# Kernel optimization log

Measured on AMD Instinct MI355X. Metric: run time of the kernel, lower is better.

Reference implementation:

```python
import jax, jax.numpy as jnp
import numpy as np

N_NODES = 50000
N_EDGES = 600000
DIM = 128
VOCAB = 512
PAD_ID = 0
LN_EPS = 1e-5


def setup_inputs() -> dict:
    key = jax.random.key(0)
    ks = jax.random.split(key, 8)
    node_ids = jax.random.randint(ks[0], (N_NODES,), 0, VOCAB, dtype=jnp.int32)
    edge_index = jax.random.randint(ks[1], (2, N_EDGES), 0, N_NODES, dtype=jnp.int32)
    edge_weight = jax.random.uniform(ks[2], (N_EDGES,), dtype=jnp.float32)
    # embedding with padding row zeroed (padding_idx semantics)
    emb = jax.random.normal(ks[3], (VOCAB, DIM), dtype=jnp.float32) * 0.05
    emb = emb.at[PAD_ID].set(0.0)
    s = 1.0 / np.sqrt(DIM)
    W1 = jax.random.normal(ks[4], (DIM, DIM), dtype=jnp.float32) * s
    b1 = jnp.zeros((DIM,), jnp.float32)
    W2 = jax.random.normal(ks[5], (DIM, DIM), dtype=jnp.float32) * s
    b2 = jnp.zeros((DIM,), jnp.float32)
    return {
        "node_ids": node_ids, "edge_index": edge_index, "edge_weight": edge_weight,
        "emb": emb, "W1": W1, "b1": b1, "W2": W2, "b2": b2,
        "gamma1": jnp.ones((DIM,), jnp.float32), "beta1": jnp.zeros((DIM,), jnp.float32),
        "gamma2": jnp.ones((DIM,), jnp.float32), "beta2": jnp.zeros((DIM,), jnp.float32),
    }


def _gcn_conv(x, row, col, ew, W, b, n_nodes):
    """PyG GCNConv: normalize=True, add_self_loops=True, improved=False.
    Aggregation j->i: edge (row=src j, col=dst i)."""
    h = x @ W  # [N, out]
    # add self loops with weight 1
    loop = jnp.arange(n_nodes, dtype=row.dtype)
    row_f = jnp.concatenate([row, loop])
    col_f = jnp.concatenate([col, loop])
    ew_f = jnp.concatenate([ew, jnp.ones((n_nodes,), ew.dtype)])
    # symmetric degree normalization (deg over destination index)
    deg = jax.ops.segment_sum(ew_f, col_f, num_segments=n_nodes)
    dis = jnp.where(deg > 0, jax.lax.rsqrt(jnp.maximum(deg, 1e-12)), 0.0)
    norm = dis[row_f] * ew_f * dis[col_f]  # [E+N]
    msg = norm[:, None] * h[row_f]  # gather + scale  [E+N, out]
    out = jax.ops.segment_sum(msg, col_f, num_segments=n_nodes)  # scatter-add
    return out + b


def _layer_norm(x, gamma, beta):
    mu = jnp.mean(x, axis=-1, keepdims=True)
    var = jnp.mean(jnp.square(x - mu), axis=-1, keepdims=True)
    return (x - mu) * jax.lax.rsqrt(var + LN_EPS) * gamma + beta


def reference(node_ids, edge_index, edge_weight, emb, W1, b1, W2, b2,
              gamma1, beta1, gamma2, beta2):
    row, col = edge_index[0], edge_index[1]
    x = emb[node_ids]  # [N, D]
    x1 = _gcn_conv(x, row, col, edge_weight, W1, b1, N_NODES)
    x = _layer_norm(x + x1, gamma1, beta1)  # dropout is identity in eval
    x2 = _gcn_conv(x, row, col, edge_weight, W2, b2, N_NODES)
    x = _layer_norm(x + x2, gamma2, beta2)
    return x
```

## Files before the change

kernel.cpp:

```cpp
#include <hip/hip_runtime.h>

#define N_NODES 50000
#define N_EDGES 600000
#define DIM     128
#define VOCAB   512
#define LN_EPS  1e-5f
#define FIX20   1048576.0f
#define WSC     65535.0f
#define BCAP    64

typedef unsigned int uint;
typedef unsigned long long ull;
typedef unsigned short ushort;
typedef __attribute__((ext_vector_type(8))) short s8v;
typedef __attribute__((ext_vector_type(4))) float f4v;
typedef __attribute__((ext_vector_type(4))) int   i4v;
typedef __attribute__((ext_vector_type(4))) float fv4;
typedef __attribute__((ext_vector_type(2))) float f2v;

__device__ __forceinline__ uint f2bf(float f) {
    uint u = __float_as_uint(f);
    return (u + 0x7fffu + ((u >> 16) & 1u)) >> 16;
}
__device__ __forceinline__ float bf_lo(uint p) { return __uint_as_float(p << 16); }
__device__ __forceinline__ float bf_hi(uint p) { return __uint_as_float(p & 0xffff0000u); }
__device__ __forceinline__ float dis_of(uint pv) {
    return rsqrtf(1.0f + (float)(pv & 0x03ffffffu) * (1.0f / FIX20));
}

__global__ __launch_bounds__(256) void deg_mm1_kernel(
        const int* __restrict__ ei, const float* __restrict__ ew,
        uint2* pairN, const int* __restrict__ nid, uint* __restrict__ epack, int E,
        const float* __restrict__ X, const float* __restrict__ W,
        uint* __restrict__ Hb, int M,
        const float* __restrict__ W2, ushort* __restrict__ Wp) {
    __shared__ float Wt[32 * 128];
    __shared__ float Xt[64 * 36];
    int tid = threadIdx.x;
    int nbDeg = (E / 4 + 255) / 256;
    int nmm = (M + 63) / 64;
    if ((int)blockIdx.x < nbDeg) {
        int e0 = (blockIdx.x * 256 + tid) * 4;
        if (e0 >= E) return;
        i4v s4 = __builtin_nontemporal_load((const i4v*)(ei + e0));
        i4v c4 = __builtin_nontemporal_load((const i4v*)(ei + E + e0));
        fv4 w4 = __builtin_nontemporal_load((const fv4*)(ew + e0));
        int   s[4] = {s4.x, s4.y, s4.z, s4.w};
        int   c[4] = {c4.x, c4.y, c4.z, c4.w};
        float w[4] = {w4.x, w4.y, w4.z, w4.w};
        uint r[4];
        #pragma unroll
        for (int k = 0; k < 4; k++) {
            uint a = (1u << 26) | (uint)__float2int_rn(w[k] * FIX20);
            r[k] = atomicAdd(&((uint*)pairN)[2 * (size_t)c[k]], a);
        }
        #pragma unroll
        for (int k = 0; k < 4; k++) {
            uint rk = r[k] >> 26;
            uint wq = (uint)__float2int_rn(w[k] * WSC);
            epack[(size_t)c[k] * BCAP + rk] = (uint)s[k] | (wq << 16);
        }
        return;
    }
    if ((int)blockIdx.x >= nbDeg + nmm) {
        int o = (blockIdx.x - nbDeg - nmm) * 256 + tid;
        if (o < 16384) {
            int j = o & 7, lane = (o >> 3) & 63, chunk = o >> 9;
            int kc = chunk & 3, nc = chunk >> 2;
            int k = kc * 32 + (lane >> 4) * 8 + j;
            int n = nc * 16 + (lane & 15);
            Wp[o] = (ushort)f2bf(W2[k * 128 + n]);
        } else {
            int i = o - 16384;
            if (i < N_NODES) ((uint*)pairN)[2 * (size_t)i + 1] = (uint)nid[i];
        }
        return;
    }
    int bx = blockIdx.x - nbDeg;
    int tx = tid & 31, ty = tid >> 5;
    int r0 = bx * 64;
    float acc[8][4];
    #pragma unroll
    for (int j = 0; j < 8; j++)
        #pragma unroll
        for (int c = 0; c < 4; c++) acc[j][c] = 0.f;

    for (int kb = 0; kb < 128; kb += 32) {
        __syncthreads();
        #pragma unroll
        for (int q = 0; q < 4; q++) {
            int f = q * 256 + tid;
            ((float4*)Wt)[f] = *(const float4*)(W + kb * 128 + f * 4);
        }
        #pragma unroll
        for (int q = 0; q < 2; q++) {
            int f = q * 256 + tid;
            int row = f >> 3, cs = f & 7;
            int gr = r0 + row;
            float4 xv = make_float4(0.f, 0.f, 0.f, 0.f);
            if (gr < M) xv = *(const float4*)(X + (size_t)gr * 128 + kb + cs * 4);
            *(float4*)(Xt + row * 36 + cs * 4) = xv;
        }
        __syncthreads();
        #pragma unroll
        for (int k = 0; k < 32; k += 4) {
            float wv[4][4];
            #pragma unroll
            for (int kk = 0; kk < 4; kk++) {
                float4 t4 = *(const float4*)(Wt + (k + kk) * 128 + tx * 4);
                wv[kk][0] = t4.x; wv[kk][1] = t4.y; wv[kk][2] = t4.z; wv[kk][3] = t4.w;
            }
            #pragma unroll
            for (int j = 0; j < 8; j++) {
                float4 xv = *(const float4*)(Xt + (ty * 8 + j) * 36 + k);
                float xs[4] = {xv.x, xv.y, xv.z, xv.w};
                #pragma unroll
                for (int kk = 0; kk < 4; kk++)
                    #pragma unroll
                    for (int c = 0; c < 4; c++)
                        acc[j][c] = fmaf(xs[kk], wv[kk][c], acc[j][c]);
            }
        }
    }
    #pragma unroll
    for (int j = 0; j < 8; j++) {
        int gr = r0 + ty * 8 + j;
        if (gr < M) {
            uint p0 = f2bf(acc[j][0]) | (f2bf(acc[j][1]) << 16);
            uint p1 = f2bf(acc[j][2]) | (f2bf(acc[j][3]) << 16);
            ((uint2*)Hb)[(size_t)gr * 32 + tx] = make_uint2(p0, p1);
        }
    }
}

__device__ __forceinline__ uint agg1_node(int i, int lane,
        const uint2* __restrict__ pairN, const uint* __restrict__ epack,
        const uint* __restrict__ hb, const float* __restrict__ emb,
        const float* __restrict__ bias, const float* __restrict__ gamma,
        const float* __restrict__ beta, uint* __restrict__ x1b) {
    int iw = __builtin_amdgcn_readfirstlane(i);
    uint2 pnw = pairN[iw];
    uint pv = pnw.x;
    int deg = (int)(pv >> 26);
    float dl = dis_of(pv);
    int hri = (int)pnw.y;
    uint ps = hb[(size_t)hri * 64 + lane];
    float slo = bf_lo(ps), shi = bf_hi(ps);
    float sx[4] = {dl * slo, 0.f, 0.f, 0.f};
    float sy[4] = {dl * shi, 0.f, 0.f, 0.f};
    const uint* ep = epack + (size_t)iw * BCAP;

    for (int j0 = 0; j0 < deg; j0 += 16) {
        uint4 rv0 = ((const uint4*)(ep + j0))[0];
        uint4 rv1 = ((const uint4*)(ep + j0))[1];
        uint4 rv2 = ((const uint4*)(ep + j0))[2];
        uint4 rv3 = ((const uint4*)(ep + j0))[3];
        uint rec[16] = {rv0.x, rv0.y, rv0.z, rv0.w,
                        rv1.x, rv1.y, rv1.z, rv1.w,
                        rv2.x, rv2.y, rv2.z, rv2.w,
                        rv3.x, rv3.y, rv3.z, rv3.w};
        uint src[16];
        #pragma unroll
        for (int k = 0; k < 16; k++)
            src[k] = (j0 + k < deg) ? (rec[k] & 0xffffu) : 0u;
        uint2 pnk[16];
        #pragma unroll
        for (int k = 0; k < 16; k++)
            pnk[k] = pairN[src[k]];
        uint qv[16];
        #pragma unroll
        for (int k = 0; k < 16; k++)
            qv[k] = hb[(size_t)pnk[k].y * 64 + lane];
        #pragma unroll
        for (int k = 0; k < 16; k++) {
            float w = (j0 + k < deg) ? (float)(rec[k] >> 16) * (1.0f / WSC) : 0.f;
            w *= rsqrtf(1.0f + (float)(pnk[k].x & 0x03ffffffu) * (1.0f / FIX20));
            sx[k & 3] += w * bf_lo(qv[k]);
            sy[k & 3] += w * bf_hi(qv[k]);
        }
    }
    float acc0 = (sx[0] + sx[1]) + (sx[2] + sx[3]);
    float acc1 = (sy[0] + sy[1]) + (sy[2] + sy[3]);
    float2 xr = ((const float2*)emb)[(size_t)hri * 64 + lane];
    float2 bi = ((const float2*)bias)[lane];
    float v0 = xr.x + dl * acc0 + bi.x;
    float v1 = xr.y + dl * acc1 + bi.y;
    float s1 = v0 + v1, s2 = v0 * v0 + v1 * v1;
    #pragma unroll
    for (int o = 32; o > 0; o >>= 1) {
        s1 += __shfl_xor(s1, o, 64);
        s2 += __shfl_xor(s2, o, 64);
    }
    float mu   = s1 * (1.0f / DIM);
    float var  = s2 * (1.0f / DIM) - mu * mu;
    float rstd = rsqrtf(var + LN_EPS);
    float2 ga = ((const float2*)gamma)[lane];
    float2 be = ((const float2*)beta)[lane];
    float o0 = (v0 - mu) * rstd * ga.x + be.x;
    float o1 = (v1 - mu) * rstd * ga.y + be.y;
    uint pw = f2bf(o0) | (f2bf(o1) << 16);
    __builtin_nontemporal_store(pw, x1b + (size_t)i * 64 + lane);
    return pw;
}

__global__ __launch_bounds__(256) void agg1_mm2(
        const uint2* __restrict__ pairN, const uint* __restrict__ epack,
        const uint* __restrict__ hembB, const ushort* __restrict__ Wp,
        const float* __restrict__ emb,
        const float* __restrict__ b1, const float* __restrict__ g1,
        const float* __restrict__ be1,
        uint* __restrict__ x1b, char* __restrict__ h8,
        float* __restrict__ rsc) {
    __shared__ uint  Xs[16][68];
    __shared__ float wmax[4][4][4];
    int tid = threadIdx.x, lane = tid & 63, wv = tid >> 6;
    int b0 = blockIdx.x * 16;

    #pragma unroll
    for (int t = 0; t < 4; t++) {
        int row = wv * 4 + t;
        uint pw = agg1_node(b0 + row, lane, pairN, epack, hembB, emb,
                            b1, g1, be1, x1b);
        Xs[row][lane] = pw;
    }
    __syncthreads();

    int quad = lane >> 4, lo = lane & 15;
    s8v a[4];
    #pragma unroll
    for (int kc = 0; kc < 4; kc++)
        a[kc] = *(const s8v*)&Xs[lo][quad * 4 + kc * 16];
    f4v acc[2];
    #pragma unroll
    for (int c = 0; c < 2; c++) {
        int nc = wv * 2 + c;
        acc[c] = (f4v){0.f, 0.f, 0.f, 0.f};
        #pragma unroll
        for (int kc = 0; kc < 4; kc++) {
            s8v b = *(const s8v*)(Wp + (size_t)((nc * 4 + kc) * 64 + lane) * 8);
            acc[c] = __builtin_amdgcn_mfma_f32_16x16x32_bf16(a[kc], b, acc[c], 0, 0, 0);
        }
    }
    float m[4];
    #pragma unroll
    for (int r = 0; r < 4; r++)
        m[r] = fmaxf(fabsf(acc[0][r]), fabsf(acc[1][r]));
    #pragma unroll
    for (int o = 1; o <= 8; o <<= 1)
        #pragma unroll
        for (int r = 0; r < 4; r++) m[r] = fmaxf(m[r], __shfl_xor(m[r], o, 64));
    if (lo == 0)
        #pragma unroll
        for (int r = 0; r < 4; r++) wmax[wv][quad][r] = m[r];
    __syncthreads();
    float fm[4];
    #pragma unroll
    for (int r = 0; r < 4; r++)
        fm[r] = fmaxf(fmaxf(wmax[0][quad][r], wmax[1][quad][r]),
                      fmaxf(wmax[2][quad][r], wmax[3][quad][r]));
    #pragma unroll
    for (int r = 0; r < 4; r++) {
        float inv = (fm[r] > 0.f) ? 127.0f / fm[r] : 0.f;
        char* hp = h8 + (size_t)(b0 + quad * 4 + r) * 128 + lo;
        #pragma unroll
        for (int c = 0; c < 2; c++)
            hp[(wv * 2 + c) * 16] = (char)__float2int_rn(acc[c][r] * inv);
    }
    if (wv == 0 && lo == 0) {
        #pragma unroll
        for (int r = 0; r < 4; r++) {
            int rr = b0 + quad * 4 + r;
            rsc[rr] = fm[r] * (1.0f / 127.0f) * dis_of(pairN[rr].x);
        }
    }
}

__global__ __launch_bounds__(256) void agg2_ln(const uint2* __restrict__ pairN,
                                               const uint* __restrict__ epack,
                                               const ushort* __restrict__ hb,
                                               const float* __restrict__ rowscale,
                                               const uint* __restrict__ resid,
                                               const float* __restrict__ bias,
                                               const float* __restrict__ gamma,
                                               const float* __restrict__ beta,
                                               float* __restrict__ out, int n) {
    int i = (blockIdx.x * 256 + threadIdx.x) >> 6;
    int lane = threadIdx.x & 63;
    if (i >= n) return;
    int iw = __builtin_amdgcn_readfirstlane(i);
    uint pv = pairN[iw].x;
    int deg = (int)(pv >> 26);
    float dl = dis_of(pv);
    uint ps = hb[(size_t)iw * 64 + lane];
    float sc0 = rowscale[iw];
    float slo = sc0 * (float)(signed char)(ps & 0xffu);
    float shi = sc0 * (float)(signed char)(ps >> 8);
    float sx[4] = {slo, 0.f, 0.f, 0.f};
    float sy[4] = {shi, 0.f, 0.f, 0.f};
    const uint* ep = epack + (size_t)iw * BCAP;

    for (int j0 = 0; j0 < deg; j0 += 16) {
        uint4 rv0 = ((const uint4*)(ep + j0))[0];
        uint4 rv1 = ((const uint4*)(ep + j0))[1];
        uint4 rv2 = ((const uint4*)(ep + j0))[2];
        uint4 rv3 = ((const uint4*)(ep + j0))[3];
        uint rec[16] = {rv0.x, rv0.y, rv0.z, rv0.w,
                        rv1.x, rv1.y, rv1.z, rv1.w,
                        rv2.x, rv2.y, rv2.z, rv2.w,
                        rv3.x, rv3.y, rv3.z, rv3.w};
        uint src[16];
        #pragma unroll
        for (int k = 0; k < 16; k++)
            src[k] = (j0 + k < deg) ? (rec[k] & 0xffffu) : 0u;
        uint qv[16];
        float scv[16];
        #pragma unroll
        for (int k = 0; k < 16; k++)
            qv[k] = hb[(size_t)src[k] * 64 + lane];
        #pragma unroll
        for (int k = 0; k < 16; k++)
            scv[k] = rowscale[src[k]];
        #pragma unroll
        for (int k = 0; k < 16; k++) {
            float w = (j0 + k < deg) ? (float)(rec[k] >> 16) * (1.0f / WSC) : 0.f;
            w *= scv[k];
            sx[k & 3] += w * (float)(signed char)(qv[k] & 0xffu);
            sy[k & 3] += w * (float)(signed char)(qv[k] >> 8);
        }
    }
    float acc0 = (sx[0] + sx[1]) + (sx[2] + sx[3]);
    float acc1 = (sy[0] + sy[1]) + (sy[2] + sy[3]);
    uint pr = __builtin_nontemporal_load(resid + (size_t)iw * 64 + lane);
    float2 bi = ((const float2*)bias)[lane];
    float v0 = bf_lo(pr) + dl * acc0 + bi.x;
    float v1 = bf_hi(pr) + dl * acc1 + bi.y;
    float s1 = v0 + v1, s2 = v0 * v0 + v1 * v1;
    #pragma unroll
    for (int o = 32; o > 0; o >>= 1) {
        s1 += __shfl_xor(s1, o, 64);
        s2 += __shfl_xor(s2, o, 64);
    }
    float mu   = s1 * (1.0f / DIM);
    float var  = s2 * (1.0f / DIM) - mu * mu;
    float rstd = rsqrtf(var + LN_EPS);
    float2 ga = ((const float2*)gamma)[lane];
    float2 be = ((const float2*)beta)[lane];
    float o0 = (v0 - mu) * rstd * ga.x + be.x;
    float o1 = (v1 - mu) * rstd * ga.y + be.y;
    f2v ov = {o0, o1};
    __builtin_nontemporal_store(ov, (f2v*)((float2*)out + (size_t)i * 64 + lane));
}

extern "C" void kernel_launch(void* const* d_in, const int* in_sizes, int n_in,
                              void* d_out, int out_size, void* d_ws, size_t ws_size,
                              hipStream_t stream) {
    const int*   node_ids = (const int*)  d_in[0];
    const int*   ei       = (const int*)  d_in[1];
    const float* ew       = (const float*)d_in[2];
    const float* emb      = (const float*)d_in[3];
    const float* W1       = (const float*)d_in[4];
    const float* b1       = (const float*)d_in[5];
    const float* W2       = (const float*)d_in[6];
    const float* b2       = (const float*)d_in[7];
    const float* g1       = (const float*)d_in[8];
    const float* be1      = (const float*)d_in[9];
    const float* g2       = (const float*)d_in[10];
    const float* be2      = (const float*)d_in[11];
    float* out = (float*)d_out;

    char* p = (char*)d_ws;
    auto alloc = [&](size_t bytes) {
        char* r = p;
        p += (bytes + 255) & ~(size_t)255;
        return r;
    };
    char*   h8      = (char*)  alloc((size_t)N_NODES * DIM);
    float*  rsc     = (float*) alloc((size_t)N_NODES * 4);
    uint*   x1b     = (uint*)  alloc((size_t)N_NODES * 64 * 4);
    uint*   hembB   = (uint*)  alloc((size_t)VOCAB * 64 * 4);
    ushort* Wp      = (ushort*)alloc((size_t)128 * 128 * 2);
    uint2*  pairN   = (uint2*) alloc((size_t)N_NODES * 8);
    uint*   epack   = (uint*)  alloc((size_t)N_NODES * BCAP * 4);

    int nbDeg = (N_EDGES / 4 + 255) / 256;
    int nmm = (VOCAB + 63) / 64;
    int nTail = 64 + (N_NODES + 255) / 256;

    (void)hipMemsetAsync(pairN, 0, (size_t)N_NODES * 8, stream);
    deg_mm1_kernel<<<nbDeg + nmm + nTail, 256, 0, stream>>>(
        ei, ew, pairN, node_ids, epack, N_EDGES, emb, W1, hembB, VOCAB, W2, Wp);

    agg1_mm2<<<N_NODES / 16, 256, 0, stream>>>(
        pairN, epack, hembB, Wp, emb, b1, g1, be1, x1b, h8, rsc);

    agg2_ln<<<(N_NODES + 3) / 4, 256, 0, stream>>>(
        pairN, epack, (const ushort*)h8, rsc, x1b, b2, g2, be2, out, N_NODES);
}
```

Before: 207.7 us.

## Widen edge records with vocab id and float weight; one node per wave in agg1

Each edge record grows to 8 bytes. It now carries the source node, that node's vocab id and the full fp32 weight. This removes the dependent per-neighbour pairN lookup before the embedding gather in the first aggregation, and drops the 16-bit weight quantisation. The interleaved degree/id array is split into a plain packed-degree array plus direct reads of node_ids, which also drops the tail blocks that copied node ids. agg1_mm2 moves to 1024-thread blocks with one node per wave, and 8 of the 16 waves each compute one 16-column MFMA tile. The trade-off is double the edge-record storage and bandwidth, plus barriers placed inside divergent branches.

```diff
diff --git a/kernel.cpp b/kernel.cpp
--- a/kernel.cpp
+++ b/kernel.cpp
@@ -6,7 +6,6 @@
 #define VOCAB   512
 #define LN_EPS  1e-5f
 #define FIX20   1048576.0f
-#define WSC     65535.0f
 #define BCAP    64
 
 typedef unsigned int uint;
@@ -30,7 +29,7 @@
 
 __global__ __launch_bounds__(256) void deg_mm1_kernel(
         const int* __restrict__ ei, const float* __restrict__ ew,
-        uint2* pairN, const int* __restrict__ nid, uint* __restrict__ epack, int E,
+        uint* pack, const int* __restrict__ nid, uint2* __restrict__ epack, int E,
         const float* __restrict__ X, const float* __restrict__ W,
         uint* __restrict__ Hb, int M,
         const float* __restrict__ W2, ushort* __restrict__ Wp) {
@@ -48,32 +47,30 @@
         int   s[4] = {s4.x, s4.y, s4.z, s4.w};
         int   c[4] = {c4.x, c4.y, c4.z, c4.w};
         float w[4] = {w4.x, w4.y, w4.z, w4.w};
+        int nv[4];
+        #pragma unroll
+        for (int k = 0; k < 4; k++) nv[k] = nid[s[k]];
         uint r[4];
         #pragma unroll
         for (int k = 0; k < 4; k++) {
             uint a = (1u << 26) | (uint)__float2int_rn(w[k] * FIX20);
-            r[k] = atomicAdd(&((uint*)pairN)[2 * (size_t)c[k]], a);
+            r[k] = atomicAdd(&pack[c[k]], a);
         }
         #pragma unroll
         for (int k = 0; k < 4; k++) {
             uint rk = r[k] >> 26;
-            uint wq = (uint)__float2int_rn(w[k] * WSC);
-            epack[(size_t)c[k] * BCAP + rk] = (uint)s[k] | (wq << 16);
+            epack[(size_t)c[k] * BCAP + rk] =
+                make_uint2((uint)s[k] | ((uint)nv[k] << 16), __float_as_uint(w[k]));
         }
         return;
     }
     if ((int)blockIdx.x >= nbDeg + nmm) {
         int o = (blockIdx.x - nbDeg - nmm) * 256 + tid;
-        if (o < 16384) {
-            int j = o & 7, lane = (o >> 3) & 63, chunk = o >> 9;
-            int kc = chunk & 3, nc = chunk >> 2;
-            int k = kc * 32 + (lane >> 4) * 8 + j;
-            int n = nc * 16 + (lane & 15);
-            Wp[o] = (ushort)f2bf(W2[k * 128 + n]);
-        } else {
-            int i = o - 16384;
-            if (i < N_NODES) ((uint*)pairN)[2 * (size_t)i + 1] = (uint)nid[i];
-        }
+        int j = o & 7, lane = (o >> 3) & 63, chunk = o >> 9;
+        int kc = chunk & 3, nc = chunk >> 2;
+        int k = kc * 32 + (lane >> 4) * 8 + j;
+        int n = nc * 16 + (lane & 15);
+        Wp[o] = (ushort)f2bf(W2[k * 128 + n]);
         return;
     }
     int bx = blockIdx.x - nbDeg;
@@ -134,47 +131,51 @@
 }
 
 __device__ __forceinline__ uint agg1_node(int i, int lane,
-        const uint2* __restrict__ pairN, const uint* __restrict__ epack,
-        const uint* __restrict__ hb, const float* __restrict__ emb,
-        const float* __restrict__ bias, const float* __restrict__ gamma,
-        const float* __restrict__ beta, uint* __restrict__ x1b) {
+        const uint* __restrict__ pack, const int* __restrict__ nid,
+        const uint2* __restrict__ epack, const uint* __restrict__ hb,
+        const float* __restrict__ emb, const float* __restrict__ bias,
+        const float* __restrict__ gamma, const float* __restrict__ beta,
+        uint* __restrict__ x1b) {
     int iw = __builtin_amdgcn_readfirstlane(i);
-    uint2 pnw = pairN[iw];
-    uint pv = pnw.x;
+    uint pv = pack[iw];
     int deg = (int)(pv >> 26);
     float dl = dis_of(pv);
-    int hri = (int)pnw.y;
+    int hri = nid[iw];
     uint ps = hb[(size_t)hri * 64 + lane];
     float slo = bf_lo(ps), shi = bf_hi(ps);
     float sx[4] = {dl * slo, 0.f, 0.f, 0.f};
     float sy[4] = {dl * shi, 0.f, 0.f, 0.f};
-    const uint* ep = epack + (size_t)iw * BCAP;
+    const uint2* ep = epack + (size_t)iw * BCAP;
 
     for (int j0 = 0; j0 < deg; j0 += 16) {
-        uint4 rv0 = ((const uint4*)(ep + j0))[0];
-        uint4 rv1 = ((const uint4*)(ep + j0))[1];
-        uint4 rv2 = ((const uint4*)(ep + j0))[2];
-        uint4 rv3 = ((const uint4*)(ep + j0))[3];
-        uint rec[16] = {rv0.x, rv0.y, rv0.z, rv0.w,
-                        rv1.x, rv1.y, rv1.z, rv1.w,
-                        rv2.x, rv2.y, rv2.z, rv2.w,
-                        rv3.x, rv3.y, rv3.z, rv3.w};
-        uint src[16];
+        const uint4* ep4 = (const uint4*)(ep + j0);
+        uint  rx[16]; float ry[16];
+        #pragma unroll
+        for (int q = 0; q < 8; q++) {
+            uint4 v = ep4[q];
+            rx[2 * q]     = v.x; ry[2 * q]     = __uint_as_float(v.y);
+            rx[2 * q + 1] = v.z; ry[2 * q + 1] = __uint_as_float(v.w);
+        }
+        uint srcv[16], hrv[16]; float wv_[16];
+        #pragma unroll
+        for (int k = 0; k < 16; k++) {
+            bool valid = (j0 + k < deg);
+            uint rxk = valid ? rx[k] : rx[0];
+            wv_[k] = valid ? ry[k] : 0.f;
+            srcv[k] = rxk & 0xffffu;
+            hrv[k]  = rxk >> 16;
+        }
+        uint pk[16];
+        #pragma unroll
+        for (int k = 0; k < 16; k++) pk[k] = pack[srcv[k]];
+        uint qv[16];
         #pragma unroll
         for (int k = 0; k < 16; k++)
-            src[k] = (j0 + k < deg) ? (rec[k] & 0xffffu) : 0u;
-        uint2 pnk[16];
-        #pragma unroll
-        for (int k = 0; k < 16; k++)
-            pnk[k] = pairN[src[k]];
-        uint qv[16];
-        #pragma unroll
-        for (int k = 0; k < 16; k++)
-            qv[k] = hb[(size_t)pnk[k].y * 64 + lane];
+            qv[k] = hb[(size_t)hrv[k] * 64 + lane];
         #pragma unroll
         for (int k = 0; k < 16; k++) {
-            float w = (j0 + k < deg) ? (float)(rec[k] >> 16) * (1.0f / WSC) : 0.f;
-            w *= rsqrtf(1.0f + (float)(pnk[k].x & 0x03ffffffu) * (1.0f / FIX20));
+            float w = wv_[k] *
+                rsqrtf(1.0f + (float)(pk[k] & 0x03ffffffu) * (1.0f / FIX20));
             sx[k & 3] += w * bf_lo(qv[k]);
             sy[k & 3] += w * bf_hi(qv[k]);
         }
@@ -203,80 +204,76 @@
     return pw;
 }
 
-__global__ __launch_bounds__(256) void agg1_mm2(
-        const uint2* __restrict__ pairN, const uint* __restrict__ epack,
-        const uint* __restrict__ hembB, const ushort* __restrict__ Wp,
-        const float* __restrict__ emb,
+__global__ __launch_bounds__(1024) void agg1_mm2(
+        const uint* __restrict__ pack, const int* __restrict__ nid,
+        const uint2* __restrict__ epack, const uint* __restrict__ hembB,
+        const ushort* __restrict__ Wp, const float* __restrict__ emb,
         const float* __restrict__ b1, const float* __restrict__ g1,
         const float* __restrict__ be1,
         uint* __restrict__ x1b, char* __restrict__ h8,
         float* __restrict__ rsc) {
     __shared__ uint  Xs[16][68];
-    __shared__ float wmax[4][4][4];
+    __shared__ float wmax[8][4][4];
     int tid = threadIdx.x, lane = tid & 63, wv = tid >> 6;
     int b0 = blockIdx.x * 16;
 
-    #pragma unroll
-    for (int t = 0; t < 4; t++) {
-        int row = wv * 4 + t;
-        uint pw = agg1_node(b0 + row, lane, pairN, epack, hembB, emb,
-                            b1, g1, be1, x1b);
-        Xs[row][lane] = pw;
-    }
+    uint pw = agg1_node(b0 + wv, lane, pack, nid, epack, hembB, emb,
+                        b1, g1, be1, x1b);
+    Xs[wv][lane] = pw;
     __syncthreads();
 
     int quad = lane >> 4, lo = lane & 15;
-    s8v a[4];
-    #pragma unroll
-    for (int kc = 0; kc < 4; kc++)
-        a[kc] = *(const s8v*)&Xs[lo][quad * 4 + kc * 16];
-    f4v acc[2];
-    #pragma unroll
-    for (int c = 0; c < 2; c++) {
-        int nc = wv * 2 + c;
-        acc[c] = (f4v){0.f, 0.f, 0.f, 0.f};
+    if (wv < 8) {
+        s8v a[4];
+        #pragma unroll
+        for (int kc = 0; kc < 4; kc++)
+            a[kc] = *(const s8v*)&Xs[lo][quad * 4 + kc * 16];
+        f4v acc = (f4v){0.f, 0.f, 0.f, 0.f};
         #pragma unroll
         for (int kc = 0; kc < 4; kc++) {
-            s8v b = *(const s8v*)(Wp + (size_t)((nc * 4 + kc) * 64 + lane) * 8);
-            acc[c] = __builtin_amdgcn_mfma_f32_16x16x32_bf16(a[kc], b, acc[c], 0, 0, 0);
-        }
-    }
-    float m[4];
-    #pragma unroll
-    for (int r = 0; r < 4; r++)
-        m[r] = fmaxf(fabsf(acc[0][r]), fabsf(acc[1][r]));
-    #pragma unroll
-    for (int o = 1; o <= 8; o <<= 1)
-        #pragma unroll
-        for (int r = 0; r < 4; r++) m[r] = fmaxf(m[r], __shfl_xor(m[r], o, 64));
-    if (lo == 0)
-        #pragma unroll
-        for (int r = 0; r < 4; r++) wmax[wv][quad][r] = m[r];
-    __syncthreads();
-    float fm[4];
-    #pragma unroll
-    for (int r = 0; r < 4; r++)
-        fm[r] = fmaxf(fmaxf(wmax[0][quad][r], wmax[1][quad][r]),
-                      fmaxf(wmax[2][quad][r], wmax[3][quad][r]));
-    #pragma unroll
-    for (int r = 0; r < 4; r++) {
-        float inv = (fm[r] > 0.f) ? 127.0f / fm[r] : 0.f;
-        char* hp = h8 + (size_t)(b0 + quad * 4 + r) * 128 + lo;
-        #pragma unroll
-        for (int c = 0; c < 2; c++)
-            hp[(wv * 2 + c) * 16] = (char)__float2int_rn(acc[c][r] * inv);
-    }
-    if (wv == 0 && lo == 0) {
+            s8v b = *(const s8v*)(Wp + (size_t)((wv * 4 + kc) * 64 + lane) * 8);
+            acc = __builtin_amdgcn_mfma_f32_16x16x32_bf16(a[kc], b, acc, 0, 0, 0);
+        }
+        float m[4];
+        #pragma unroll
+        for (int r = 0; r < 4; r++) m[r] = fabsf(acc[r]);
+        #pragma unroll
+        for (int o = 1; o <= 8; o <<= 1)
+            #pragma unroll
+            for (int r = 0; r < 4; r++) m[r] = fmaxf(m[r], __shfl_xor(m[r], o, 64));
+        if (lo == 0)
+            #pragma unroll
+            for (int r = 0; r < 4; r++) wmax[wv][quad][r] = m[r];
+        __syncthreads();
+        float fm[4];
         #pragma unroll
         for (int r = 0; r < 4; r++) {
-            int rr = b0 + quad * 4 + r;
-            rsc[rr] = fm[r] * (1.0f / 127.0f) * dis_of(pairN[rr].x);
-        }
-    }
-}
-
-__global__ __launch_bounds__(256) void agg2_ln(const uint2* __restrict__ pairN,
-                                               const uint* __restrict__ epack,
+            float a01 = fmaxf(wmax[0][quad][r], wmax[1][quad][r]);
+            float a23 = fmaxf(wmax[2][quad][r], wmax[3][quad][r]);
+            float a45 = fmaxf(wmax[4][quad][r], wmax[5][quad][r]);
+            float a67 = fmaxf(wmax[6][quad][r], wmax[7][quad][r]);
+            fm[r] = fmaxf(fmaxf(a01, a23), fmaxf(a45, a67));
+        }
+        #pragma unroll
+        for (int r = 0; r < 4; r++) {
+            float inv = (fm[r] > 0.f) ? 127.0f / fm[r] : 0.f;
+            h8[(size_t)(b0 + quad * 4 + r) * 128 + wv * 16 + lo] =
+                (char)__float2int_rn(acc[r] * inv);
+        }
+        if (wv == 0 && lo == 0) {
+            #pragma unroll
+            for (int r = 0; r < 4; r++) {
+                int rr = b0 + quad * 4 + r;
+                rsc[rr] = fm[r] * (1.0f / 127.0f) * dis_of(pack[rr]);
+            }
+        }
+    } else {
+        __syncthreads();
+    }
+}
+
+__global__ __launch_bounds__(256) void agg2_ln(const uint* __restrict__ pack,
+                                               const uint2* __restrict__ epack,
                                                const ushort* __restrict__ hb,
                                                const float* __restrict__ rowscale,
                                                const uint* __restrict__ resid,
@@ -288,7 +285,7 @@
     int lane = threadIdx.x & 63;
     if (i >= n) return;
     int iw = __builtin_amdgcn_readfirstlane(i);
-    uint pv = pairN[iw].x;
+    uint pv = pack[iw];
     int deg = (int)(pv >> 26);
     float dl = dis_of(pv);
     uint ps = hb[(size_t)iw * 64 + lane];
@@ -297,33 +294,35 @@
     float shi = sc0 * (float)(signed char)(ps >> 8);
     float sx[4] = {slo, 0.f, 0.f, 0.f};
     float sy[4] = {shi, 0.f, 0.f, 0.f};
-    const uint* ep = epack + (size_t)iw * BCAP;
+    const uint2* ep = epack + (size_t)iw * BCAP;
 
     for (int j0 = 0; j0 < deg; j0 += 16) {
-        uint4 rv0 = ((const uint4*)(ep + j0))[0];
-        uint4 rv1 = ((const uint4*)(ep + j0))[1];
-        uint4 rv2 = ((const uint4*)(ep + j0))[2];
-        uint4 rv3 = ((const uint4*)(ep + j0))[3];
-        uint rec[16] = {rv0.x, rv0.y, rv0.z, rv0.w,
-                        rv1.x, rv1.y, rv1.z, rv1.w,
-                        rv2.x, rv2.y, rv2.z, rv2.w,
-                        rv3.x, rv3.y, rv3.z, rv3.w};
-        uint src[16];
+        const uint4* ep4 = (const uint4*)(ep + j0);
+        uint  rx[16]; float ry[16];
+        #pragma unroll
+        for (int q = 0; q < 8; q++) {
+            uint4 v = ep4[q];
+            rx[2 * q]     = v.x; ry[2 * q]     = __uint_as_float(v.y);
+            rx[2 * q + 1] = v.z; ry[2 * q + 1] = __uint_as_float(v.w);
+        }
+        uint srcv[16]; float wv_[16];
+        #pragma unroll
+        for (int k = 0; k < 16; k++) {
+            bool valid = (j0 + k < deg);
+            srcv[k] = (valid ? rx[k] : rx[0]) & 0xffffu;
+            wv_[k] = valid ? ry[k] : 0.f;
+        }
+        uint qv[16];
         #pragma unroll
         for (int k = 0; k < 16; k++)
-            src[k] = (j0 + k < deg) ? (rec[k] & 0xffffu) : 0u;
-        uint qv[16];
+            qv[k] = hb[(size_t)srcv[k] * 64 + lane];
         float scv[16];
         #pragma unroll
         for (int k = 0; k < 16; k++)
-            qv[k] = hb[(size_t)src[k] * 64 + lane];
-        #pragma unroll
-        for (int k = 0; k < 16; k++)
-            scv[k] = rowscale[src[k]];
+            scv[k] = rowscale[srcv[k]];
         #pragma unroll
         for (int k = 0; k < 16; k++) {
-            float w = (j0 + k < deg) ? (float)(rec[k] >> 16) * (1.0f / WSC) : 0.f;
-            w *= scv[k];
+            float w = wv_[k] * scv[k];
             sx[k & 3] += w * (float)(signed char)(qv[k] & 0xffu);
             sy[k & 3] += w * (float)(signed char)(qv[k] >> 8);
         }
@@ -379,20 +378,20 @@
     uint*   x1b     = (uint*)  alloc((size_t)N_NODES * 64 * 4);
     uint*   hembB   = (uint*)  alloc((size_t)VOCAB * 64 * 4);
     ushort* Wp      = (ushort*)alloc((size_t)128 * 128 * 2);
-    uint2*  pairN   = (uint2*) alloc((size_t)N_NODES * 8);
-    uint*   epack   = (uint*)  alloc((size_t)N_NODES * BCAP * 4);
+    uint*   pack    = (uint*)  alloc((size_t)N_NODES * 4);
+    uint2*  epack   = (uint2*) alloc((size_t)N_NODES * BCAP * 8);
 
     int nbDeg = (N_EDGES / 4 + 255) / 256;
     int nmm = (VOCAB + 63) / 64;
-    int nTail = 64 + (N_NODES + 255) / 256;
-
-    (void)hipMemsetAsync(pairN, 0, (size_t)N_NODES * 8, stream);
+    int nTail = 64;
+
+    (void)hipMemsetAsync(pack, 0, (size_t)N_NODES * 4, stream);
     deg_mm1_kernel<<<nbDeg + nmm + nTail, 256, 0, stream>>>(
-        ei, ew, pairN, node_ids, epack, N_EDGES, emb, W1, hembB, VOCAB, W2, Wp);
-
-    agg1_mm2<<<N_NODES / 16, 256, 0, stream>>>(
-        pairN, epack, hembB, Wp, emb, b1, g1, be1, x1b, h8, rsc);
+        ei, ew, pack, node_ids, epack, N_EDGES, emb, W1, hembB, VOCAB, W2, Wp);
+
+    agg1_mm2<<<N_NODES / 16, 1024, 0, stream>>>(
+        pack, node_ids, epack, hembB, Wp, emb, b1, g1, be1, x1b, h8, rsc);
 
     agg2_ln<<<(N_NODES + 3) / 4, 256, 0, stream>>>(
-        pairN, epack, (const ushort*)h8, rsc, x1b, b2, g2, be2, out, N_NODES);
-}
+        pack, epack, (const ushort*)h8, rsc, x1b, b2, g2, be2, out, N_NODES);
+}
```

New measurement: 236.4 us. +13.8%, slower.
